# Performance work log

Measured on AMD Instinct MI355X. Metric: run time of the kernel, lower is better.

## Reference

```python
import jax, jax.numpy as jnp
import numpy as np

N_BLOCKS = 8
BLOCK = 512
HIDDEN = N_BLOCKS * BLOCK  # 4096


def setup_inputs() -> dict:
    key = jax.random.key(0)
    k1, k2 = jax.random.split(key)
    x = jax.random.normal(k1, (4, 4096, HIDDEN), dtype=jnp.float32)
    # per-sub-transform matrices (what trans.get_matrix(inv_t) would return)
    blocks = jax.random.normal(k2, (N_BLOCKS, BLOCK, BLOCK), dtype=jnp.float32)
    return {"x": x, "blocks": blocks}


def reference(x, blocks):
    # Original: matrix = block_diag(*blocks); out = x.reshape(-1, H) @ matrix
    # Block-diagonal structure means each hidden slice of size BLOCK only
    # multiplies its own block -> grouped GEMM, identical math, no zeros.
    init_shape = x.shape
    xr = x.reshape(-1, N_BLOCKS, BLOCK)  # [tokens, k, b]
    out = jnp.einsum("nkb,kbc->nkc", xr, blocks)
    return out.reshape(init_shape)
```

## Files before the change

kernel.cpp:

```cpp
#include <hip/hip_runtime.h>
#include <stdint.h>


#define HID 4096
#define KD  512
#define NKB 8
#define BM  128
#define BN  128
#define BK  32
#define MTILES 128
#define ASTRIDE 40

typedef __attribute__((ext_vector_type(4))) float    f32x4;
typedef __attribute__((ext_vector_type(8))) short    s16x8;
typedef __attribute__((ext_vector_type(4))) uint32_t u32x4;

__device__ uint16_t g_bt[(size_t)NKB * KD * KD];

__device__ __forceinline__ void async_copy16(const void* g, void* l) {
  __builtin_amdgcn_global_load_lds((const __attribute__((address_space(1))) void*)g,
                                   (__attribute__((address_space(3))) void*)l,
                                   16, 0, 0);
}

__device__ __forceinline__ uint16_t f2bf_rne(float f) {
  uint32_t u = __float_as_uint(f);
  u += 0x7fffu + ((u >> 16) & 1u);
  return (uint16_t)(u >> 16);
}

__global__ void convert_blocks_k(const float* __restrict__ blocks) {
  __shared__ float tile[32][33];
  const int kb = blockIdx.z;
  const int c0 = blockIdx.x * 32;
  const int b0 = blockIdx.y * 32;
  const int tx = threadIdx.x;
  const int ty = threadIdx.y;
  const float* src = blocks + ((size_t)kb * KD + b0) * KD + c0;
#pragma unroll
  for (int i = 0; i < 4; ++i) {
    const int r = ty + i * 8;
    tile[r][tx] = src[(size_t)r * KD + tx];
  }
  __syncthreads();
  uint16_t* dst = g_bt + ((size_t)kb * KD + c0) * KD + b0;
#pragma unroll
  for (int i = 0; i < 4; ++i) {
    const int r = ty + i * 8;
    dst[(size_t)r * KD + tx] = f2bf_rne(tile[tx][r]);
  }
}

__global__ void grouped_gemm_k(const float* __restrict__ x, float* __restrict__ out) {
  __shared__ uint16_t lA[BM * ASTRIDE];
  __shared__ uint16_t lB[BN * BK];

  const int tid = threadIdx.x;
  const int wg  = blockIdx.x;
  const int nt  =  wg       & 3;
  const int kb  = (wg >> 2) & 7;
  const int mt  =  wg >> 5;

  const int wave = tid >> 6;
  const int lane = tid & 63;
  const int ln   = lane & 15;
  const int qd   = lane >> 4;
  const int wm   = (wave & 1) * 64;
  const int wn   = (wave >> 1) * 64;

  const int am = tid >> 1;
  const int ah = tid & 1;
  const float* aptr = x + (size_t)(mt * BM + am) * HID + kb * KD + ah * 16;
  uint16_t* awr = lA + am * ASTRIDE + ah * 16;

  const int bn0 = tid >> 2;
  const int bs0 = (tid & 3) ^ (bn0 & 3) ^ ((bn0 >> 2) & 3);
  const int p1  = tid + 256;
  const int bn1 = p1 >> 2;
  const int bs1 = (p1 & 3) ^ (bn1 & 3) ^ ((bn1 >> 2) & 3);
  const uint16_t* bsrc0 = g_bt + (size_t)(kb * KD + nt * BN + bn0) * KD + bs0 * 8;
  const uint16_t* bsrc1 = g_bt + (size_t)(kb * KD + nt * BN + bn1) * KD + bs1 * 8;
  uint16_t* bdst0 = lB + tid * 8;
  uint16_t* bdst1 = lB + p1 * 8;

  const int sw = (ln & 3) ^ ((ln >> 2) & 3);
  const uint16_t* ard = lA + (wm + ln) * ASTRIDE + qd * 8;
  const uint16_t* brd = lB + ((wn + ln) * 4 + (qd ^ sw)) * 8;

  f32x4 acc[4][4];
#pragma unroll
  for (int mi = 0; mi < 4; ++mi)
#pragma unroll
    for (int ni = 0; ni < 4; ++ni)
      acc[mi][ni] = (f32x4){0.f, 0.f, 0.f, 0.f};

  for (int kk = 0; kk < KD / BK; ++kk) {
    const int k0 = kk * BK;
    const f32x4 a0 = *(const f32x4*)(aptr + k0);
    const f32x4 a1 = *(const f32x4*)(aptr + k0 + 4);
    const f32x4 a2 = *(const f32x4*)(aptr + k0 + 8);
    const f32x4 a3 = *(const f32x4*)(aptr + k0 + 12);

    __syncthreads();

    async_copy16(bsrc0 + k0, bdst0);
    async_copy16(bsrc1 + k0, bdst1);

    u32x4 w0, w1;
    w0.x = __builtin_amdgcn_perm(__float_as_uint(a0.y), __float_as_uint(a0.x), 0x07060302u);
    w0.y = __builtin_amdgcn_perm(__float_as_uint(a0.w), __float_as_uint(a0.z), 0x07060302u);
    w0.z = __builtin_amdgcn_perm(__float_as_uint(a1.y), __float_as_uint(a1.x), 0x07060302u);
    w0.w = __builtin_amdgcn_perm(__float_as_uint(a1.w), __float_as_uint(a1.z), 0x07060302u);
    w1.x = __builtin_amdgcn_perm(__float_as_uint(a2.y), __float_as_uint(a2.x), 0x07060302u);
    w1.y = __builtin_amdgcn_perm(__float_as_uint(a2.w), __float_as_uint(a2.z), 0x07060302u);
    w1.z = __builtin_amdgcn_perm(__float_as_uint(a3.y), __float_as_uint(a3.x), 0x07060302u);
    w1.w = __builtin_amdgcn_perm(__float_as_uint(a3.w), __float_as_uint(a3.z), 0x07060302u);
    *(u32x4*)(awr)     = w0;
    *(u32x4*)(awr + 8) = w1;

    __syncthreads();

    s16x8 af[4], bf[4];
#pragma unroll
    for (int mi = 0; mi < 4; ++mi) af[mi] = *(const s16x8*)(ard + mi * (16 * ASTRIDE));
#pragma unroll
    for (int ni = 0; ni < 4; ++ni) bf[ni] = *(const s16x8*)(brd + ni * (16 * 32));
#pragma unroll
    for (int mi = 0; mi < 4; ++mi)
#pragma unroll
      for (int ni = 0; ni < 4; ++ni)
        acc[mi][ni] = __builtin_amdgcn_mfma_f32_16x16x32_bf16(af[mi], bf[ni], acc[mi][ni], 0, 0, 0);
  }

  const int col = kb * KD + nt * BN + wn + ln;
#pragma unroll
  for (int mi = 0; mi < 4; ++mi) {
    const int row0 = mt * BM + wm + mi * 16 + qd * 4;
#pragma unroll
    for (int r = 0; r < 4; ++r) {
      float* orow = out + (size_t)(row0 + r) * HID + col;
#pragma unroll
      for (int ni = 0; ni < 4; ++ni)
        orow[ni * 16] = acc[mi][ni][r];
    }
  }
}

extern "C" void kernel_launch(void* const* d_in, const int* in_sizes, int n_in,
                              void* d_out, int out_size, void* d_ws, size_t ws_size,
                              hipStream_t stream) {
  const float* x      = (const float*)d_in[0];
  const float* blocks = (const float*)d_in[1];
  float* out = (float*)d_out;
  (void)d_ws; (void)ws_size; (void)in_sizes; (void)n_in; (void)out_size;

  convert_blocks_k<<<dim3(16, 16, 8), dim3(32, 8, 1), 0, stream>>>(blocks);
  grouped_gemm_k<<<dim3(MTILES * NKB * 4, 1, 1), dim3(256, 1, 1), 0, stream>>>(x, out);
}
```

Before: 554.5 us.

## Double-buffer LDS tiles, stage epilogue through LDS, remap block order

Adds ping-pong LDS buffers so the global loads and async copies for the next K-step are issued before the MFMAs of the current step, which halves the barriers per iteration. The epilogue now stages accumulators through LDS so each lane writes 16-byte contiguous rows instead of scattered scalar stores. It also remaps block IDs with a stride-of-8 interleave and adds launch bounds. The cost is twice the LDS footprint, more registers held across the loop for the prefetched A values, and an extra LDS round trip in the epilogue.

```diff
diff --git a/kernel.cpp b/kernel.cpp
--- a/kernel.cpp
+++ b/kernel.cpp
@@ -10,6 +10,9 @@
 #define BK  32
 #define MTILES 128
 #define ASTRIDE 40
+#define LAHALF (BM * ASTRIDE)
+#define LBHALF (BN * BK)
+#define NIT (KD / BK)
 
 typedef __attribute__((ext_vector_type(4))) float    f32x4;
 typedef __attribute__((ext_vector_type(8))) short    s16x8;
@@ -51,15 +54,18 @@
   }
 }
 
-__global__ void grouped_gemm_k(const float* __restrict__ x, float* __restrict__ out) {
-  __shared__ uint16_t lA[BM * ASTRIDE];
-  __shared__ uint16_t lB[BN * BK];
+__global__ void __launch_bounds__(256, 4)
+grouped_gemm_k(const float* __restrict__ x, float* __restrict__ out) {
+  __shared__ uint16_t smem[2 * LAHALF + 2 * LBHALF];
+  uint16_t* lA = smem;
+  uint16_t* lB = smem + 2 * LAHALF;
 
   const int tid = threadIdx.x;
-  const int wg  = blockIdx.x;
-  const int nt  =  wg       & 3;
-  const int kb  = (wg >> 2) & 7;
-  const int mt  =  wg >> 5;
+  const int bid = blockIdx.x;
+  const int j   = (bid & 7) * (MTILES * NKB * 4 / 8) + (bid >> 3);
+  const int nt  =  j       & 3;
+  const int kb  = (j >> 2) & 7;
+  const int mt  =  j >> 5;
 
   const int wave = tid >> 6;
   const int lane = tid & 63;
@@ -94,18 +100,13 @@
     for (int ni = 0; ni < 4; ++ni)
       acc[mi][ni] = (f32x4){0.f, 0.f, 0.f, 0.f};
 
-  for (int kk = 0; kk < KD / BK; ++kk) {
-    const int k0 = kk * BK;
-    const f32x4 a0 = *(const f32x4*)(aptr + k0);
-    const f32x4 a1 = *(const f32x4*)(aptr + k0 + 4);
-    const f32x4 a2 = *(const f32x4*)(aptr + k0 + 8);
-    const f32x4 a3 = *(const f32x4*)(aptr + k0 + 12);
-
-    __syncthreads();
-
-    async_copy16(bsrc0 + k0, bdst0);
-    async_copy16(bsrc1 + k0, bdst1);
-
+  {
+    async_copy16(bsrc0, bdst0);
+    async_copy16(bsrc1, bdst1);
+    const f32x4 a0 = *(const f32x4*)(aptr);
+    const f32x4 a1 = *(const f32x4*)(aptr + 4);
+    const f32x4 a2 = *(const f32x4*)(aptr + 8);
+    const f32x4 a3 = *(const f32x4*)(aptr + 12);
     u32x4 w0, w1;
     w0.x = __builtin_amdgcn_perm(__float_as_uint(a0.y), __float_as_uint(a0.x), 0x07060302u);
     w0.y = __builtin_amdgcn_perm(__float_as_uint(a0.w), __float_as_uint(a0.z), 0x07060302u);
@@ -117,31 +118,69 @@
     w1.w = __builtin_amdgcn_perm(__float_as_uint(a3.w), __float_as_uint(a3.z), 0x07060302u);
     *(u32x4*)(awr)     = w0;
     *(u32x4*)(awr + 8) = w1;
+  }
 
+  for (int k = 0; k < NIT; ++k) {
+    const int cur = k & 1;
+    const int nxt = cur ^ 1;
     __syncthreads();
 
+    f32x4 a0, a1, a2, a3;
+    if (k < NIT - 1) {
+      const int k1 = (k + 1) * BK;
+      async_copy16(bsrc0 + k1, bdst0 + nxt * LBHALF);
+      async_copy16(bsrc1 + k1, bdst1 + nxt * LBHALF);
+      a0 = *(const f32x4*)(aptr + k1);
+      a1 = *(const f32x4*)(aptr + k1 + 4);
+      a2 = *(const f32x4*)(aptr + k1 + 8);
+      a3 = *(const f32x4*)(aptr + k1 + 12);
+    }
+
+    const uint16_t* ar = ard + cur * LAHALF;
+    const uint16_t* br = brd + cur * LBHALF;
     s16x8 af[4], bf[4];
 #pragma unroll
-    for (int mi = 0; mi < 4; ++mi) af[mi] = *(const s16x8*)(ard + mi * (16 * ASTRIDE));
+    for (int mi = 0; mi < 4; ++mi) af[mi] = *(const s16x8*)(ar + mi * (16 * ASTRIDE));
 #pragma unroll
-    for (int ni = 0; ni < 4; ++ni) bf[ni] = *(const s16x8*)(brd + ni * (16 * 32));
+    for (int ni = 0; ni < 4; ++ni) bf[ni] = *(const s16x8*)(br + ni * (16 * 32));
 #pragma unroll
     for (int mi = 0; mi < 4; ++mi)
 #pragma unroll
       for (int ni = 0; ni < 4; ++ni)
         acc[mi][ni] = __builtin_amdgcn_mfma_f32_16x16x32_bf16(af[mi], bf[ni], acc[mi][ni], 0, 0, 0);
+
+    if (k < NIT - 1) {
+      u32x4 w0, w1;
+      w0.x = __builtin_amdgcn_perm(__float_as_uint(a0.y), __float_as_uint(a0.x), 0x07060302u);
+      w0.y = __builtin_amdgcn_perm(__float_as_uint(a0.w), __float_as_uint(a0.z), 0x07060302u);
+      w0.z = __builtin_amdgcn_perm(__float_as_uint(a1.y), __float_as_uint(a1.x), 0x07060302u);
+      w0.w = __builtin_amdgcn_perm(__float_as_uint(a1.w), __float_as_uint(a1.z), 0x07060302u);
+      w1.x = __builtin_amdgcn_perm(__float_as_uint(a2.y), __float_as_uint(a2.x), 0x07060302u);
+      w1.y = __builtin_amdgcn_perm(__float_as_uint(a2.w), __float_as_uint(a2.z), 0x07060302u);
+      w1.z = __builtin_amdgcn_perm(__float_as_uint(a3.y), __float_as_uint(a3.x), 0x07060302u);
+      w1.w = __builtin_amdgcn_perm(__float_as_uint(a3.w), __float_as_uint(a3.z), 0x07060302u);
+      *(u32x4*)(awr + nxt * LAHALF)     = w0;
+      *(u32x4*)(awr + nxt * LAHALF + 8) = w1;
+    }
   }
 
-  const int col = kb * KD + nt * BN + wn + ln;
+  __syncthreads();
+  float* eb = (float*)smem + wave * (16 * 68);
+  const int rr = lane >> 4;
+  const int cs = (lane & 15) * 4;
+  const int colb = kb * KD + nt * BN + wn + cs;
 #pragma unroll
   for (int mi = 0; mi < 4; ++mi) {
-    const int row0 = mt * BM + wm + mi * 16 + qd * 4;
 #pragma unroll
-    for (int r = 0; r < 4; ++r) {
-      float* orow = out + (size_t)(row0 + r) * HID + col;
+    for (int ni = 0; ni < 4; ++ni)
 #pragma unroll
-      for (int ni = 0; ni < 4; ++ni)
-        orow[ni * 16] = acc[mi][ni][r];
+      for (int r = 0; r < 4; ++r)
+        eb[(qd * 4 + r) * 68 + ln + ni * 16] = acc[mi][ni][r];
+#pragma unroll
+    for (int sub = 0; sub < 4; ++sub) {
+      const f32x4 v = *(const f32x4*)(eb + (sub * 4 + rr) * 68 + cs);
+      const int row = mt * BM + wm + mi * 16 + sub * 4 + rr;
+      *(f32x4*)(out + (size_t)row * HID + colb) = v;
     }
   }
 }
```

Measured after the change: 568.0 us. 2.4% more time.
